# Kernel optimization log

Hardware: AMD Instinct MI355X
Metric: run time of the kernel (lower is better)

The kernel has to match this reference:

```python
import jax, jax.numpy as jnp
import numpy as np
from jax import lax

NUM_WORDS, WORD_DIM = 50000, 300
NUM_CHARS, CHAR_DIM = 100, 100
NUM_POS, POS_DIM = 50, 100
NUM_FILTERS, KERNEL = 100, 3
PRIVACY_TERMS = (3, 7, 11)


def setup_inputs() -> dict:
    key = jax.random.key(0)
    ks = jax.random.split(key, 8)
    bs, ls, cl = 64, 512, 32
    return {
        "input_word": jax.random.randint(ks[0], (bs, ls), 0, NUM_WORDS, dtype=jnp.int64 if jax.config.jax_enable_x64 else jnp.int32),
        "input_char": jax.random.randint(ks[1], (bs, ls, cl), 0, NUM_CHARS),
        "input_pos": jax.random.randint(ks[2], (bs, ls), 0, NUM_POS),
        "word_table": jax.random.normal(ks[3], (NUM_WORDS, WORD_DIM), jnp.float32) * 0.1,
        "char_table": jax.random.normal(ks[4], (NUM_CHARS, CHAR_DIM), jnp.float32) * 0.1,
        "pos_table": jax.random.normal(ks[5], (NUM_POS, POS_DIM), jnp.float32) * 0.1,
        "conv_w": jax.random.normal(ks[6], (NUM_FILTERS, CHAR_DIM, KERNEL), jnp.float32) * 0.05,
        "conv_b": jax.random.normal(ks[7], (NUM_FILTERS,), jnp.float32) * 0.05,
    }


def _dist_feature(input_pos):
    # nearest-privacy-token distance: parallel prefix-min via cummax/cummin scans
    priv = jnp.asarray(PRIVACY_TERMS)
    pri_mask = (input_pos[..., None] == priv).any(-1)           # [bs, ls]
    ls = input_pos.shape[1]
    pos_idx = jnp.arange(ls)                                      # [ls]
    last = lax.cummax(jnp.where(pri_mask, pos_idx, -1000), axis=1)                 # last privacy idx <= j
    nxt = lax.cummin(jnp.where(pri_mask, pos_idx, 1000), axis=1, reverse=True)     # next privacy idx >= j
    dis = jnp.minimum(pos_idx - last, nxt - pos_idx).astype(jnp.float32)
    return dis[..., None]                                         # [bs, ls, 1]


def _char_cnn(char_emb, conv_w, conv_b):
    # char_emb: [bs, ls, cl, char_dim] -> [bs, ls, num_filters]
    bs, ls, cl, cd = char_emb.shape
    x = char_emb.reshape(bs * ls, cl, cd).transpose(0, 2, 1)      # [N, C, L]
    y = lax.conv_general_dilated(x, conv_w, window_strides=(1,),
                                 padding=[(KERNEL - 1, KERNEL - 1)],
                                 dimension_numbers=("NCH", "OIH", "NCH"))
    y = y + conv_b[None, :, None]
    y = jnp.tanh(y.max(axis=2))                                   # max over length, then tanh
    return y.reshape(bs, ls, -1)


def reference(input_word, input_char, input_pos, word_table, char_table, pos_table, conv_w, conv_b):
    dis = _dist_feature(input_pos)
    word = word_table[input_word]                                 # [bs, ls, word_dim]
    char = _char_cnn(char_table[input_char], conv_w, conv_b)      # [bs, ls, num_filters]
    pos = pos_table[input_pos]                                    # [bs, ls, pos_dim]
    return jnp.concatenate([dis, word, char, pos], axis=2)
```

## Files before the change

### kernel.cpp

```cpp
#include <hip/hip_runtime.h>
#include <hip/hip_fp16.h>

#define BS 64
#define LS 512
#define CL 32
#define WD 300
#define NC 100
#define CD 100
#define PD 100
#define NF 100
#define KK 3
#define OPAD8 128
#define PROW8 (KK*OPAD8)
#define PBYTES8 (NC*PROW8)
#define NV4_8 (PBYTES8/16)
#define OUTD 501
#define TPB 64
#define NTHR 1024

typedef _Float16 h2 __attribute__((ext_vector_type(2)));
typedef float f32x2 __attribute__((ext_vector_type(2)));

template <bool HI>
__device__ __forceinline__ h2 cvt2(unsigned w) {
    f32x2 f = __builtin_amdgcn_cvt_pk_f32_fp8((int)w, HI);
    return __builtin_bit_cast(h2, __builtin_amdgcn_cvt_pkrtz(f.x, f.y));
}

__global__ void precompute_P(const float* __restrict__ conv_w,
                             const float* __restrict__ char_table,
                             unsigned char* __restrict__ P) {
    const int c = blockIdx.x;
    const int k = blockIdx.y;
    const int o = threadIdx.x;
    __shared__ float row[CD];
    if (o < CD) row[o] = char_table[c * CD + o];
    __syncthreads();
    float acc = 0.f;
    if (o < NF) {
        const float* w = conv_w + o * (CD * KK) + k;
        #pragma unroll 4
        for (int i = 0; i < CD; ++i) acc += w[i * KK] * row[i];
    }
    const int enc = __builtin_amdgcn_cvt_pk_fp8_f32(acc, 0.f, 0, false);
    P[(c * KK + k) * OPAD8 + o] = (unsigned char)(enc & 0xFF);
}

#define TAP(i, W0, W1, W2, HI)                                          \
    {                                                                   \
        const h2 p0 = cvt2<HI>(W0);                                     \
        const h2 p1 = cvt2<HI>(W1);                                     \
        const h2 p2 = cvt2<HI>(W2);                                     \
        const h2 y = a0[i] + p2;                                        \
        m[i]  = __builtin_elementwise_max(m[i], y);                     \
        a0[i] = a1[i] + p1;                                             \
        a1[i] = p0;                                                     \
    }

__global__ __launch_bounds__(NTHR, 8) void main_kernel(
        const int* __restrict__ input_word,
        const int* __restrict__ input_char,
        const int* __restrict__ input_pos,
        const float* __restrict__ word_table,
        const float* __restrict__ pos_table,
        const float* __restrict__ conv_b,
        const unsigned char* __restrict__ Pg,
        float* __restrict__ out) {
    __shared__ alignas(16) unsigned char Pl[PBYTES8];
    __shared__ alignas(16) unsigned char s_char[TPB * CL];
    __shared__ unsigned long long s_mask[LS / 64];

    const int tid  = threadIdx.x;
    const int tok0 = blockIdx.x * TPB;

    const uint4* src = (const uint4*)Pg;
    const uint4 s0 = src[tid];
    const uint4 s1 = src[tid + NTHR];
    uint4 s2 = {};
    const bool h2nd = tid < (NV4_8 - 2 * NTHR);
    if (h2nd) s2 = src[tid + 2 * NTHR];

    if (tid < LS) {
        const int p = input_pos[(tok0 >> 9) * LS + tid];
        const bool pm = (p == 3) | (p == 7) | (p == 11);
        const unsigned long long b = __ballot(pm);
        if ((tid & 63) == 0) s_mask[tid >> 6] = b;
    }

    if (tid < (TPB * CL) / 4) {
        const int4 c4 = ((const int4*)(input_char + tok0 * CL))[tid];
        ((unsigned*)s_char)[tid] =
            (unsigned)c4.x | ((unsigned)c4.y << 8) | ((unsigned)c4.z << 16) | ((unsigned)c4.w << 24);
    }

    {
        uint4* dst = (uint4*)Pl;
        dst[tid] = s0;
        dst[tid + NTHR] = s1;
        if (h2nd) dst[tid + 2 * NTHR] = s2;
    }
    __syncthreads();

    if (tid < 512) {
        const int wid  = tid >> 6;
        const int lane = tid & 63;
        const int l    = lane & 15;
        const char* Pb = (const char*)Pl + l * 8;
        const unsigned* s_cw = (const unsigned*)s_char;

        #pragma unroll 1
        for (int pass = 0; pass < 2; ++pass) {
            const int tb = wid * 8 + pass * 4 + (lane >> 4);
            h2 a0[4], a1[4], m[4];
            #pragma unroll
            for (int i = 0; i < 4; ++i) {
                a0[i] = (h2)(_Float16)0;
                a1[i] = (h2)(_Float16)0;
                m[i]  = (h2)(_Float16)(-60000.f);
            }
            #pragma unroll 1
            for (int w = 0; w < CL / 4; ++w) {
                const unsigned wd = s_cw[tb * (CL / 4) + w];
                #pragma unroll
                for (int b = 0; b < 4; ++b) {
                    const int ca = (int)((wd >> (8 * b)) & 0xFFu) * PROW8;
                    const uint2 q0 = *(const uint2*)(Pb + ca + 0 * OPAD8);
                    const uint2 q1 = *(const uint2*)(Pb + ca + 1 * OPAD8);
                    const uint2 q2 = *(const uint2*)(Pb + ca + 2 * OPAD8);
                    TAP(0, q0.x, q1.x, q2.x, false)
                    TAP(1, q0.x, q1.x, q2.x, true)
                    TAP(2, q0.y, q1.y, q2.y, false)
                    TAP(3, q0.y, q1.y, q2.y, true)
                }
            }
            if (l < 13) {
                float mm[8];
                #pragma unroll
                for (int i = 0; i < 4; ++i) {
                    const h2 v = __builtin_elementwise_max(m[i], __builtin_elementwise_max(a0[i], a1[i]));
                    mm[2 * i]     = (float)v.x;
                    mm[2 * i + 1] = (float)v.y;
                }
                const float4 b0 = *(const float4*)(conv_b + 8 * l);
                float* outc = out + (size_t)(tok0 + tb) * OUTD + 301 + 8 * l;
                outc[0] = tanhf(mm[0] + b0.x);
                outc[1] = tanhf(mm[1] + b0.y);
                outc[2] = tanhf(mm[2] + b0.z);
                outc[3] = tanhf(mm[3] + b0.w);
                if (l < 12) {
                    const float4 b1 = *(const float4*)(conv_b + 8 * l + 4);
                    outc[4] = tanhf(mm[4] + b1.x);
                    outc[5] = tanhf(mm[5] + b1.y);
                    outc[6] = tanhf(mm[6] + b1.z);
                    outc[7] = tanhf(mm[7] + b1.w);
                }
            }
        }

        for (int i = tid; i < TPB * (PD / 4); i += 512) {
            const int t = i / (PD / 4);
            const int j = i - t * (PD / 4);
            const int p = input_pos[tok0 + t];
            const float4 v = ((const float4*)pos_table)[p * (PD / 4) + j];
            float* o = out + (size_t)(tok0 + t) * OUTD + 401 + 4 * j;
            o[0] = v.x; o[1] = v.y; o[2] = v.z; o[3] = v.w;
        }

        if (tid < TPB) {
            const int j = (tok0 & (LS - 1)) + tid;
            const int wj = j >> 6, bj = j & 63;
            int last = -1000;
            {
                unsigned long long x = s_mask[wj] & ((2ull << bj) - 1ull);
                int w = wj;
                while (true) {
                    if (x) { last = w * 64 + 63 - __clzll(x); break; }
                    if (--w < 0) break;
                    x = s_mask[w];
                }
            }
            int nxt = 1000;
            {
                unsigned long long x = s_mask[wj] & (~0ull << bj);
                int w = wj;
                while (true) {
                    if (x) { nxt = w * 64 + (int)__ffsll((long long)x) - 1; break; }
                    if (++w >= LS / 64) break;
                    x = s_mask[w];
                }
            }
            out[(size_t)(tok0 + tid) * OUTD] = (float)min(j - last, nxt - j);
        }
    } else {
        const int t2 = tid - 512;

        #pragma unroll 4
        for (int i = t2; i < TPB * (WD / 4); i += 512) {
            const int t = i / (WD / 4);
            const int j = i - t * (WD / 4);
            const int w = input_word[tok0 + t];
            const float4 v = ((const float4*)word_table)[(size_t)w * (WD / 4) + j];
            float* o = out + (size_t)(tok0 + t) * OUTD + 1 + 4 * j;
            o[0] = v.x; o[1] = v.y; o[2] = v.z; o[3] = v.w;
        }
    }
}

extern "C" void kernel_launch(void* const* d_in, const int* in_sizes, int n_in,
                              void* d_out, int out_size, void* d_ws, size_t ws_size,
                              hipStream_t stream) {
    const int*   input_word = (const int*)d_in[0];
    const int*   input_char = (const int*)d_in[1];
    const int*   input_pos  = (const int*)d_in[2];
    const float* word_table = (const float*)d_in[3];
    const float* char_table = (const float*)d_in[4];
    const float* pos_table  = (const float*)d_in[5];
    const float* conv_w     = (const float*)d_in[6];
    const float* conv_b     = (const float*)d_in[7];
    float* out = (float*)d_out;

    unsigned char* P = (unsigned char*)d_ws;

    precompute_P<<<dim3(NC, KK), 128, 0, stream>>>(conv_w, char_table, P);
    main_kernel<<<(BS * LS) / TPB, NTHR, 0, stream>>>(
        input_word, input_char, input_pos, word_table, pos_table, conv_b, P, out);
}
```

Measured before the change: 44.52 us.

## Assign one token per wave for aligned vector word/pos copies, move pos to copy waves

The word and position embedding copies are restructured so each copy wave handles one token at a time. Each wave uses 16-byte aligned vector stores into the odd-stride output row, with unaligned source loads and scalar head/tail fixups done by two lanes. The pos_table copy moves from the conv waves to the copy waves so the two halves of the block are better balanced. Per-token serial scalar loops on single lanes add some divergence overhead.

```diff
diff --git a/kernel.cpp b/kernel.cpp
--- a/kernel.cpp
+++ b/kernel.cpp
@@ -20,6 +20,8 @@
 
 typedef _Float16 h2 __attribute__((ext_vector_type(2)));
 typedef float f32x2 __attribute__((ext_vector_type(2)));
+typedef float f4u __attribute__((ext_vector_type(4), aligned(4)));
+typedef float f4a __attribute__((ext_vector_type(4), aligned(16)));
 
 template <bool HI>
 __device__ __forceinline__ h2 cvt2(unsigned w) {
@@ -72,6 +74,8 @@
 
     const int tid  = threadIdx.x;
     const int tok0 = blockIdx.x * TPB;
+    const int wid  = tid >> 6;
+    const int lane = tid & 63;
 
     const uint4* src = (const uint4*)Pg;
     const uint4 s0 = src[tid];
@@ -84,7 +88,7 @@
         const int p = input_pos[(tok0 >> 9) * LS + tid];
         const bool pm = (p == 3) | (p == 7) | (p == 11);
         const unsigned long long b = __ballot(pm);
-        if ((tid & 63) == 0) s_mask[tid >> 6] = b;
+        if (lane == 0) s_mask[wid] = b;
     }
 
     if (tid < (TPB * CL) / 4) {
@@ -102,9 +106,7 @@
     __syncthreads();
 
     if (tid < 512) {
-        const int wid  = tid >> 6;
-        const int lane = tid & 63;
-        const int l    = lane & 15;
+        const int l = lane & 15;
         const char* Pb = (const char*)Pl + l * 8;
         const unsigned* s_cw = (const unsigned*)s_char;
 
@@ -157,15 +159,6 @@
             }
         }
 
-        for (int i = tid; i < TPB * (PD / 4); i += 512) {
-            const int t = i / (PD / 4);
-            const int j = i - t * (PD / 4);
-            const int p = input_pos[tok0 + t];
-            const float4 v = ((const float4*)pos_table)[p * (PD / 4) + j];
-            float* o = out + (size_t)(tok0 + t) * OUTD + 401 + 4 * j;
-            o[0] = v.x; o[1] = v.y; o[2] = v.z; o[3] = v.w;
-        }
-
         if (tid < TPB) {
             const int j = (tok0 & (LS - 1)) + tid;
             const int wj = j >> 6, bj = j & 63;
@@ -192,16 +185,45 @@
             out[(size_t)(tok0 + tid) * OUTD] = (float)min(j - last, nxt - j);
         }
     } else {
-        const int t2 = tid - 512;
-
-        #pragma unroll 4
-        for (int i = t2; i < TPB * (WD / 4); i += 512) {
-            const int t = i / (WD / 4);
-            const int j = i - t * (WD / 4);
-            const int w = input_word[tok0 + t];
-            const float4 v = ((const float4*)word_table)[(size_t)w * (WD / 4) + j];
-            float* o = out + (size_t)(tok0 + t) * OUTD + 1 + 4 * j;
-            o[0] = v.x; o[1] = v.y; o[2] = v.z; o[3] = v.w;
+        const int cw = wid - 8;
+
+        #pragma unroll 2
+        for (int tk = 0; tk < 8; ++tk) {
+            const int t    = cw * 8 + tk;
+            const int base = (tok0 + t) * OUTD;
+
+            const int w = __builtin_amdgcn_readfirstlane(input_word[tok0 + t]);
+            const float* srcw = word_table + (size_t)w * WD;
+            const int g0 = (base + 4) & ~3;
+            const int h  = g0 - (base + 1);
+            const int n  = (base + 301 - g0) >> 2;
+            if (lane < n)
+                *(f4a*)(out + g0 + 4 * lane) = *(const f4u*)(srcw + h + 4 * lane);
+            if (lane + 64 < n)
+                *(f4a*)(out + g0 + 4 * (lane + 64)) = *(const f4u*)(srcw + h + 4 * (lane + 64));
+
+            const int p = __builtin_amdgcn_readfirstlane(input_pos[tok0 + t]);
+            const float* srcp = pos_table + p * PD;
+            const int gp = (base + 404) & ~3;
+            const int hp = gp - (base + 401);
+            const int np = (base + 501 - gp) >> 2;
+            if (lane < np)
+                *(f4a*)(out + gp + 4 * lane) = *(const f4u*)(srcp + hp + 4 * lane);
+
+            if (lane == 62) {
+                #pragma unroll 1
+                for (int i = 0; i < h; ++i) out[base + 1 + i] = srcw[i];
+                const int r = 300 - h - 4 * n;
+                #pragma unroll 1
+                for (int i = 0; i < r; ++i) out[g0 + 4 * n + i] = srcw[h + 4 * n + i];
+            }
+            if (lane == 63) {
+                #pragma unroll 1
+                for (int i = 0; i < hp; ++i) out[base + 401 + i] = srcp[i];
+                const int rp = 100 - hp - 4 * np;
+                #pragma unroll 1
+                for (int i = 0; i < rp; ++i) out[gp + 4 * np + i] = srcp[hp + 4 * np + i];
+            }
         }
     }
 }
```

New measurement: 56.80 us. 27.6% more time.

## Halve block size and drop warp specialization in main kernel

Applied to the files above, without the earlier changes.

Blocks now handle 32 tokens with 512 threads instead of 64 tokens with 1024. Every thread does one char-CNN token-slice and then takes part in the word, pos and distance gathers, replacing the split where half the threads ran the CNN and half copied word embeddings. The fp8 P table is still copied into shared memory per block, and since there are twice as many blocks, total shared-memory fill traffic doubles. The aim is better load balance and more blocks in flight, at the cost of serialising the CNN phase before the gathers within each block.

```diff
diff --git a/kernel.cpp b/kernel.cpp
--- a/kernel.cpp
+++ b/kernel.cpp
@@ -15,8 +15,8 @@
 #define PBYTES8 (NC*PROW8)
 #define NV4_8 (PBYTES8/16)
 #define OUTD 501
-#define TPB 64
-#define NTHR 1024
+#define TPB 32
+#define NTHR 512
 
 typedef _Float16 h2 __attribute__((ext_vector_type(2)));
 typedef float f32x2 __attribute__((ext_vector_type(2)));
@@ -57,7 +57,7 @@
         a1[i] = p0;                                                     \
     }
 
-__global__ __launch_bounds__(NTHR, 8) void main_kernel(
+__global__ __launch_bounds__(NTHR, 6) void main_kernel(
         const int* __restrict__ input_word,
         const int* __restrict__ input_char,
         const int* __restrict__ input_pos,
@@ -72,16 +72,17 @@
 
     const int tid  = threadIdx.x;
     const int tok0 = blockIdx.x * TPB;
-
-    const uint4* src = (const uint4*)Pg;
-    const uint4 s0 = src[tid];
-    const uint4 s1 = src[tid + NTHR];
-    uint4 s2 = {};
-    const bool h2nd = tid < (NV4_8 - 2 * NTHR);
-    if (h2nd) s2 = src[tid + 2 * NTHR];
-
-    if (tid < LS) {
-        const int p = input_pos[(tok0 >> 9) * LS + tid];
+    const int row  = tok0 >> 9;
+
+    {
+        const uint4* src = (const uint4*)Pg;
+        uint4* dst = (uint4*)Pl;
+        #pragma unroll 2
+        for (int i = tid; i < NV4_8; i += NTHR) dst[i] = src[i];
+    }
+
+    {
+        const int p = input_pos[row * LS + tid];
         const bool pm = (p == 3) | (p == 7) | (p == 11);
         const unsigned long long b = __ballot(pm);
         if ((tid & 63) == 0) s_mask[tid >> 6] = b;
@@ -92,117 +93,104 @@
         ((unsigned*)s_char)[tid] =
             (unsigned)c4.x | ((unsigned)c4.y << 8) | ((unsigned)c4.z << 16) | ((unsigned)c4.w << 24);
     }
+    __syncthreads();
 
     {
-        uint4* dst = (uint4*)Pl;
-        dst[tid] = s0;
-        dst[tid + NTHR] = s1;
-        if (h2nd) dst[tid + 2 * NTHR] = s2;
-    }
-    __syncthreads();
-
-    if (tid < 512) {
-        const int wid  = tid >> 6;
-        const int lane = tid & 63;
-        const int l    = lane & 15;
+        const int tb = tid >> 4;
+        const int l  = tid & 15;
         const char* Pb = (const char*)Pl + l * 8;
         const unsigned* s_cw = (const unsigned*)s_char;
 
+        h2 a0[4], a1[4], m[4];
+        #pragma unroll
+        for (int i = 0; i < 4; ++i) {
+            a0[i] = (h2)(_Float16)0;
+            a1[i] = (h2)(_Float16)0;
+            m[i]  = (h2)(_Float16)(-60000.f);
+        }
         #pragma unroll 1
-        for (int pass = 0; pass < 2; ++pass) {
-            const int tb = wid * 8 + pass * 4 + (lane >> 4);
-            h2 a0[4], a1[4], m[4];
+        for (int w = 0; w < CL / 4; ++w) {
+            const unsigned wd = s_cw[tb * (CL / 4) + w];
+            #pragma unroll
+            for (int b = 0; b < 4; ++b) {
+                const int ca = (int)((wd >> (8 * b)) & 0xFFu) * PROW8;
+                const uint2 q0 = *(const uint2*)(Pb + ca + 0 * OPAD8);
+                const uint2 q1 = *(const uint2*)(Pb + ca + 1 * OPAD8);
+                const uint2 q2 = *(const uint2*)(Pb + ca + 2 * OPAD8);
+                TAP(0, q0.x, q1.x, q2.x, false)
+                TAP(1, q0.x, q1.x, q2.x, true)
+                TAP(2, q0.y, q1.y, q2.y, false)
+                TAP(3, q0.y, q1.y, q2.y, true)
+            }
+        }
+        if (l < 13) {
+            float mm[8];
             #pragma unroll
             for (int i = 0; i < 4; ++i) {
-                a0[i] = (h2)(_Float16)0;
-                a1[i] = (h2)(_Float16)0;
-                m[i]  = (h2)(_Float16)(-60000.f);
-            }
-            #pragma unroll 1
-            for (int w = 0; w < CL / 4; ++w) {
-                const unsigned wd = s_cw[tb * (CL / 4) + w];
-                #pragma unroll
-                for (int b = 0; b < 4; ++b) {
-                    const int ca = (int)((wd >> (8 * b)) & 0xFFu) * PROW8;
-                    const uint2 q0 = *(const uint2*)(Pb + ca + 0 * OPAD8);
-                    const uint2 q1 = *(const uint2*)(Pb + ca + 1 * OPAD8);
-                    const uint2 q2 = *(const uint2*)(Pb + ca + 2 * OPAD8);
-                    TAP(0, q0.x, q1.x, q2.x, false)
-                    TAP(1, q0.x, q1.x, q2.x, true)
-                    TAP(2, q0.y, q1.y, q2.y, false)
-                    TAP(3, q0.y, q1.y, q2.y, true)
-                }
-            }
-            if (l < 13) {
-                float mm[8];
-                #pragma unroll
-                for (int i = 0; i < 4; ++i) {
-                    const h2 v = __builtin_elementwise_max(m[i], __builtin_elementwise_max(a0[i], a1[i]));
-                    mm[2 * i]     = (float)v.x;
-                    mm[2 * i + 1] = (float)v.y;
-                }
-                const float4 b0 = *(const float4*)(conv_b + 8 * l);
-                float* outc = out + (size_t)(tok0 + tb) * OUTD + 301 + 8 * l;
-                outc[0] = tanhf(mm[0] + b0.x);
-                outc[1] = tanhf(mm[1] + b0.y);
-                outc[2] = tanhf(mm[2] + b0.z);
-                outc[3] = tanhf(mm[3] + b0.w);
-                if (l < 12) {
-                    const float4 b1 = *(const float4*)(conv_b + 8 * l + 4);
-                    outc[4] = tanhf(mm[4] + b1.x);
-                    outc[5] = tanhf(mm[5] + b1.y);
-                    outc[6] = tanhf(mm[6] + b1.z);
-                    outc[7] = tanhf(mm[7] + b1.w);
-                }
-            }
-        }
-
-        for (int i = tid; i < TPB * (PD / 4); i += 512) {
-            const int t = i / (PD / 4);
-            const int j = i - t * (PD / 4);
-            const int p = input_pos[tok0 + t];
-            const float4 v = ((const float4*)pos_table)[p * (PD / 4) + j];
-            float* o = out + (size_t)(tok0 + t) * OUTD + 401 + 4 * j;
-            o[0] = v.x; o[1] = v.y; o[2] = v.z; o[3] = v.w;
-        }
-
-        if (tid < TPB) {
-            const int j = (tok0 & (LS - 1)) + tid;
-            const int wj = j >> 6, bj = j & 63;
-            int last = -1000;
-            {
-                unsigned long long x = s_mask[wj] & ((2ull << bj) - 1ull);
-                int w = wj;
-                while (true) {
-                    if (x) { last = w * 64 + 63 - __clzll(x); break; }
-                    if (--w < 0) break;
-                    x = s_mask[w];
-                }
-            }
-            int nxt = 1000;
-            {
-                unsigned long long x = s_mask[wj] & (~0ull << bj);
-                int w = wj;
-                while (true) {
-                    if (x) { nxt = w * 64 + (int)__ffsll((long long)x) - 1; break; }
-                    if (++w >= LS / 64) break;
-                    x = s_mask[w];
-                }
-            }
-            out[(size_t)(tok0 + tid) * OUTD] = (float)min(j - last, nxt - j);
-        }
-    } else {
-        const int t2 = tid - 512;
-
-        #pragma unroll 4
-        for (int i = t2; i < TPB * (WD / 4); i += 512) {
-            const int t = i / (WD / 4);
-            const int j = i - t * (WD / 4);
-            const int w = input_word[tok0 + t];
-            const float4 v = ((const float4*)word_table)[(size_t)w * (WD / 4) + j];
-            float* o = out + (size_t)(tok0 + t) * OUTD + 1 + 4 * j;
-            o[0] = v.x; o[1] = v.y; o[2] = v.z; o[3] = v.w;
-        }
+                const h2 v = __builtin_elementwise_max(m[i], __builtin_elementwise_max(a0[i], a1[i]));
+                mm[2 * i]     = (float)v.x;
+                mm[2 * i + 1] = (float)v.y;
+            }
+            const float4 b0 = *(const float4*)(conv_b + 8 * l);
+            float* outc = out + (size_t)(tok0 + tb) * OUTD + 301 + 8 * l;
+            outc[0] = tanhf(mm[0] + b0.x);
+            outc[1] = tanhf(mm[1] + b0.y);
+            outc[2] = tanhf(mm[2] + b0.z);
+            outc[3] = tanhf(mm[3] + b0.w);
+            if (l < 12) {
+                const float4 b1 = *(const float4*)(conv_b + 8 * l + 4);
+                outc[4] = tanhf(mm[4] + b1.x);
+                outc[5] = tanhf(mm[5] + b1.y);
+                outc[6] = tanhf(mm[6] + b1.z);
+                outc[7] = tanhf(mm[7] + b1.w);
+            }
+        }
+    }
+
+    #pragma unroll 2
+    for (int i = tid; i < TPB * (WD / 4); i += NTHR) {
+        const int t = i / (WD / 4);
+        const int j = i - t * (WD / 4);
+        const int w = input_word[tok0 + t];
+        const float4 v = ((const float4*)word_table)[(size_t)w * (WD / 4) + j];
+        float* o = out + (size_t)(tok0 + t) * OUTD + 1 + 4 * j;
+        o[0] = v.x; o[1] = v.y; o[2] = v.z; o[3] = v.w;
+    }
+
+    #pragma unroll 2
+    for (int i = tid; i < TPB * (PD / 4); i += NTHR) {
+        const int t = i / (PD / 4);
+        const int j = i - t * (PD / 4);
+        const int p = input_pos[tok0 + t];
+        const float4 v = ((const float4*)pos_table)[p * (PD / 4) + j];
+        float* o = out + (size_t)(tok0 + t) * OUTD + 401 + 4 * j;
+        o[0] = v.x; o[1] = v.y; o[2] = v.z; o[3] = v.w;
+    }
+
+    if (tid < TPB) {
+        const int j = (tok0 & (LS - 1)) + tid;
+        const int wj = j >> 6, bj = j & 63;
+        int last = -1000;
+        {
+            unsigned long long x = s_mask[wj] & ((2ull << bj) - 1ull);
+            int w = wj;
+            while (true) {
+                if (x) { last = w * 64 + 63 - __clzll(x); break; }
+                if (--w < 0) break;
+                x = s_mask[w];
+            }
+        }
+        int nxt = 1000;
+        {
+            unsigned long long x = s_mask[wj] & (~0ull << bj);
+            int w = wj;
+            while (true) {
+                if (x) { nxt = w * 64 + (int)__ffsll((long long)x) - 1; break; }
+                if (++w >= LS / 64) break;
+                x = s_mask[w];
+            }
+        }
+        out[(size_t)(tok0 + tid) * OUTD] = (float)min(j - last, nxt - j);
     }
 }
 
```

New measurement: 45.24 us. Within noise of the previous version (+1.6%).
